# Performance work log

Hardware: AMD Instinct MI355X
Metric: run time of the kernel (lower is better)

Reference implementation:

```python
import jax, jax.numpy as jnp
import numpy as np

B, T, N, K = 1024, 4096, 2048, 16
M = 1 << K  # per-neuron memory size (use_hashing=False -> 2**k)


def setup_inputs() -> dict:
    key = jax.random.key(0)
    k1, k2, k3 = jax.random.split(key, 3)
    input_bits = jax.random.randint(k1, (B, T), 0, 2, dtype=jnp.int32)          # 0/1 bits
    connections = jax.random.randint(k2, (N, K), 0, T, dtype=jnp.int32)         # fixed wiring
    memory = jax.random.randint(k3, (N, M), 0, 256, dtype=jnp.int32)            # per-neuron RAM contents
    return {"input_bits": input_bits, "connections": connections, "memory": memory}


def reference(input_bits, connections, memory):
    # gather the k wired bits for every neuron: [B, N, K]
    gathered = input_bits[:, connections].astype(jnp.int32)
    # bit weights = powers of two (RAMNeuron._bit_weights), LSB-first
    bit_weights = (jnp.int32(1) << jnp.arange(K, dtype=jnp.int32))              # [K]
    # weighted sum -> memory address per (sample, neuron): [B, N]
    addresses = jnp.sum(gathered * bit_weights, axis=-1)
    # per-neuron memory lookup: memory[n, addresses[b, n]] -> [B, N]
    mems = memory[jnp.arange(N)[None, :], addresses]
    # output is the stored LSB as a bool bit
    return (mems & 1).astype(jnp.bool_)
```

## Files before the change

kernel.cpp:

```cpp
#include <hip/hip_runtime.h>
#include <cstdint>

#define Bc 1024
#define Tc 4096
#define Nc 2048
#define Kc 16
#define Mc 65536

__global__ __launch_bounds__(256) void ram_lookup_kernel(
    const int* __restrict__ input_bits,
    const int* __restrict__ connections,
    const int* __restrict__ memory,
    int* __restrict__ out)
{
    __shared__ uint32_t bits[Tc / 32];

    const int b    = blockIdx.x;
    const int tid  = threadIdx.x;
    const int lane = tid & 63;
    const int wave = tid >> 6;

    const int* row = input_bits + (size_t)b * Tc;

#pragma unroll
    for (int i = 0; i < Tc / 256; ++i) {
        const int pos = i * 256 + wave * 64 + lane;
        const unsigned long long m = __ballot(row[pos] & 1);
        if (lane == 0) {
            const int w64 = i * 4 + wave;
            bits[w64 * 2]     = (uint32_t)m;
            bits[w64 * 2 + 1] = (uint32_t)(m >> 32);
        }
    }
    __syncthreads();

    uint32_t addrs[Nc / 256];
#pragma unroll
    for (int i = 0; i < Nc / 256; ++i) {
        const int n = i * 256 + tid;
        const int4* cp = (const int4*)(connections + n * Kc);
        const int4 c0 = cp[0], c1 = cp[1], c2 = cp[2], c3 = cp[3];
        const int c[16] = {c0.x, c0.y, c0.z, c0.w,
                           c1.x, c1.y, c1.z, c1.w,
                           c2.x, c2.y, c2.z, c2.w,
                           c3.x, c3.y, c3.z, c3.w};
        uint32_t a = 0;
#pragma unroll
        for (int k = 0; k < 16; ++k) {
            const uint32_t t = (uint32_t)c[k];
            a |= ((bits[t >> 5] >> (t & 31)) & 1u) << k;
        }
        addrs[i] = a;
    }

    int vals[Nc / 256];
#pragma unroll
    for (int i = 0; i < Nc / 256; ++i) {
        const int n = i * 256 + tid;
        vals[i] = memory[(size_t)n * Mc + addrs[i]];
    }

#pragma unroll
    for (int i = 0; i < Nc / 256; ++i) {
        out[(size_t)b * Nc + i * 256 + tid] = vals[i] & 1;
    }
}

extern "C" void kernel_launch(void* const* d_in, const int* in_sizes, int n_in,
                              void* d_out, int out_size, void* d_ws, size_t ws_size,
                              hipStream_t stream) {
    const int* input_bits  = (const int*)d_in[0];
    const int* connections = (const int*)d_in[1];
    const int* memory      = (const int*)d_in[2];
    int* out               = (int*)d_out;

    hipLaunchKernelGGL(ram_lookup_kernel, dim3(Bc), dim3(256), 0, stream,
                       input_bits, connections, memory, out);
}
```

Measured before the change: 637.7 us.

## Bit-pack memory LSBs into workspace before lookups to shrink gather footprint

Measured after the change: 727.7 us. 14.1% more time.

```diff
diff --git a/kernel.cpp b/kernel.cpp
--- a/kernel.cpp
+++ b/kernel.cpp
@@ -6,11 +6,30 @@
 #define Nc 2048
 #define Kc 16
 #define Mc 65536
+#define ROW_WORDS (Mc / 32)
+#define PACKED_WORDS ((size_t)Nc * ROW_WORDS)
 
-__global__ __launch_bounds__(256) void ram_lookup_kernel(
+__global__ __launch_bounds__(256) void pack_kernel(
+    const int* __restrict__ memory, uint32_t* __restrict__ packed)
+{
+    const size_t w = (size_t)blockIdx.x * 256 + threadIdx.x;
+    const int4* src = (const int4*)(memory + w * 32);
+    uint32_t bw = 0;
+#pragma unroll
+    for (int i = 0; i < 8; ++i) {
+        const int4 v = src[i];
+        bw |= (uint32_t)(v.x & 1) << (i * 4);
+        bw |= (uint32_t)(v.y & 1) << (i * 4 + 1);
+        bw |= (uint32_t)(v.z & 1) << (i * 4 + 2);
+        bw |= (uint32_t)(v.w & 1) << (i * 4 + 3);
+    }
+    packed[w] = bw;
+}
+
+__global__ __launch_bounds__(256) void ram_lookup_packed(
     const int* __restrict__ input_bits,
     const int* __restrict__ connections,
-    const int* __restrict__ memory,
+    const uint32_t* __restrict__ packedmem,
     int* __restrict__ out)
 {
     __shared__ uint32_t bits[Tc / 32];
@@ -53,13 +72,62 @@
         addrs[i] = a;
     }
 
+    uint32_t words[Nc / 256];
+#pragma unroll
+    for (int i = 0; i < Nc / 256; ++i) {
+        const int n = i * 256 + tid;
+        words[i] = packedmem[((size_t)n << 11) + (addrs[i] >> 5)];
+    }
+
+#pragma unroll
+    for (int i = 0; i < Nc / 256; ++i) {
+        out[(size_t)b * Nc + i * 256 + tid] = (int)((words[i] >> (addrs[i] & 31)) & 1u);
+    }
+}
+
+__global__ __launch_bounds__(256) void ram_lookup_direct(
+    const int* __restrict__ input_bits,
+    const int* __restrict__ connections,
+    const int* __restrict__ memory,
+    int* __restrict__ out)
+{
+    __shared__ uint32_t bits[Tc / 32];
+    const int b = blockIdx.x, tid = threadIdx.x;
+    const int lane = tid & 63, wave = tid >> 6;
+    const int* row = input_bits + (size_t)b * Tc;
+#pragma unroll
+    for (int i = 0; i < Tc / 256; ++i) {
+        const int pos = i * 256 + wave * 64 + lane;
+        const unsigned long long m = __ballot(row[pos] & 1);
+        if (lane == 0) {
+            const int w64 = i * 4 + wave;
+            bits[w64 * 2] = (uint32_t)m;
+            bits[w64 * 2 + 1] = (uint32_t)(m >> 32);
+        }
+    }
+    __syncthreads();
+    uint32_t addrs[Nc / 256];
+#pragma unroll
+    for (int i = 0; i < Nc / 256; ++i) {
+        const int n = i * 256 + tid;
+        const int4* cp = (const int4*)(connections + n * Kc);
+        const int4 c0 = cp[0], c1 = cp[1], c2 = cp[2], c3 = cp[3];
+        const int c[16] = {c0.x, c0.y, c0.z, c0.w, c1.x, c1.y, c1.z, c1.w,
+                           c2.x, c2.y, c2.z, c2.w, c3.x, c3.y, c3.z, c3.w};
+        uint32_t a = 0;
+#pragma unroll
+        for (int k = 0; k < 16; ++k) {
+            const uint32_t t = (uint32_t)c[k];
+            a |= ((bits[t >> 5] >> (t & 31)) & 1u) << k;
+        }
+        addrs[i] = a;
+    }
     int vals[Nc / 256];
 #pragma unroll
     for (int i = 0; i < Nc / 256; ++i) {
         const int n = i * 256 + tid;
         vals[i] = memory[(size_t)n * Mc + addrs[i]];
     }
-
 #pragma unroll
     for (int i = 0; i < Nc / 256; ++i) {
         out[(size_t)b * Nc + i * 256 + tid] = vals[i] & 1;
@@ -74,6 +142,14 @@
     const int* memory      = (const int*)d_in[2];
     int* out               = (int*)d_out;
 
-    hipLaunchKernelGGL(ram_lookup_kernel, dim3(Bc), dim3(256), 0, stream,
-                       input_bits, connections, memory, out);
+    if (ws_size >= PACKED_WORDS * sizeof(uint32_t)) {
+        uint32_t* packed = (uint32_t*)d_ws;
+        hipLaunchKernelGGL(pack_kernel, dim3(PACKED_WORDS / 256), dim3(256), 0, stream,
+                           memory, packed);
+        hipLaunchKernelGGL(ram_lookup_packed, dim3(Bc), dim3(256), 0, stream,
+                           input_bits, connections, packed, out);
+    } else {
+        hipLaunchKernelGGL(ram_lookup_direct, dim3(Bc), dim3(256), 0, stream,
+                           input_bits, connections, memory, out);
+    }
 }
```
